# Kernel tuning notes

Hardware: AMD Instinct MI355X
Metric: run time of the kernel (lower is better)

The kernel has to match this reference:

```python
import jax, jax.numpy as jnp
import numpy as np

D_MODEL = 512
D_STATE = 64
LN_EPS = 1e-3  # Keras LayerNormalization default epsilon


def setup_inputs() -> dict:
    key = jax.random.key(0)
    ks = jax.random.split(key, 12)
    B, S, D, N = 8, 4096, D_MODEL, D_STATE

    def glorot(k, shape):
        fan_in, fan_out = shape[0], shape[1]
        lim = np.sqrt(6.0 / (fan_in + fan_out)).astype(np.float32)
        return jax.random.uniform(k, shape, jnp.float32, -lim, lim)

    return {
        "x": jax.random.normal(ks[0], (B, S, D), jnp.float32),
        "ln_gamma": jnp.ones((D,), jnp.float32),
        "ln_beta": jnp.zeros((D,), jnp.float32),
        "W_in": glorot(ks[1], (D, D)),
        "b_in": jnp.zeros((D,), jnp.float32),
        "W_xs": glorot(ks[2], (D, N)),
        "W_B": glorot(ks[3], (D, N)),
        "b_B": jnp.zeros((N,), jnp.float32),
        "W_C": glorot(ks[4], (D, N)),
        "b_C": jnp.zeros((N,), jnp.float32),
        "A_log": jax.random.uniform(ks[5], (N,), jnp.float32, -4.0, -1.0),
        "D_skip": jnp.ones((D,), jnp.float32),
        "W_so": glorot(ks[6], (N, D)),
        "W_out": glorot(ks[7], (D, D)),
        "b_out": jnp.zeros((D,), jnp.float32),
    }


def reference(x, ln_gamma, ln_beta, W_in, b_in, W_xs, W_B, b_B, W_C, b_C,
              A_log, D_skip, W_so, W_out, b_out):
    residual = x
    # LayerNorm over last axis (Keras default eps=1e-3)
    mu = jnp.mean(x, axis=-1, keepdims=True)
    var = jnp.mean(jnp.square(x - mu), axis=-1, keepdims=True)
    xn = (x - mu) * jax.lax.rsqrt(var + LN_EPS) * ln_gamma + ln_beta
    # input projection (this projected x is what feeds the D skip too)
    xp = xn @ W_in + b_in                      # [B, S, D]
    Bmat = xp @ W_B + b_B                      # [B, S, N] selective B(x)
    Cmat = xp @ W_C + b_C                      # [B, S, N] selective C(x)
    xs = xp @ W_xs                             # [B, S, N]
    A_bar = jnp.exp(-jnp.exp(A_log))           # [N], stable decay in (0,1)
    Bx = Bmat * xs                             # per-step drive B_t * x_state_t

    # sequential scan: h_t = A_bar * h_{t-1} + Bx_t
    def step(h, bx):
        h = A_bar * h + bx
        return h, h

    h0 = jnp.zeros((x.shape[0], A_log.shape[0]), x.dtype)
    _, hs = jax.lax.scan(step, h0, jnp.swapaxes(Bx, 0, 1))  # hs: [S, B, N]
    hs = jnp.swapaxes(hs, 0, 1)                             # [B, S, N]

    y = jnp.einsum('bsn,nd->bsd', Cmat * hs, W_so) + D_skip * xp
    y = y @ W_out + b_out
    # dropout is identity at inference (training=None)
    return y + residual
```

## Files before the change

kernel.cpp:

```cpp
#include <hip/hip_runtime.h>
#include <cstdint>
#include <cstddef>


typedef unsigned short bf16_t;
typedef __attribute__((ext_vector_type(8))) short bh8;
typedef __attribute__((ext_vector_type(4))) float f4;

#define M_ROWS 32768
#define SCAN_L 32
#define SCAN_C 128

__device__ __forceinline__ unsigned short f2bf(float f) {
  union { float f; unsigned int u; } c; c.f = f;
  unsigned int u = c.u;
  return (unsigned short)((u + 0x7FFFu + ((u >> 16) & 1u)) >> 16);
}

__device__ __forceinline__ uint2 pack4bf(f4 a) {
  uint2 r;
  r.x = (unsigned)f2bf(a[0]) | ((unsigned)f2bf(a[1]) << 16);
  r.y = (unsigned)f2bf(a[2]) | ((unsigned)f2bf(a[3]) << 16);
  return r;
}

__device__ __forceinline__ void async_cp16(void* lds, const void* g) {
  __builtin_amdgcn_global_load_lds((const __attribute__((address_space(1))) void*)g,
                                   (__attribute__((address_space(3))) void*)lds, 16, 0, 0);
}

__global__ __launch_bounds__(256) void prep_all(
    const float* __restrict__ W_in, const float* __restrict__ W_out,
    const float* __restrict__ W_so, const float* __restrict__ W_xs,
    const float* __restrict__ W_B,  const float* __restrict__ W_C,
    const float* __restrict__ b_in, const float* __restrict__ D_skip,
    const float* __restrict__ A_log,
    bf16_t* __restrict__ Wbig, bf16_t* __restrict__ Wout_t,
    bf16_t* __restrict__ Win_b, bf16_t* __restrict__ Wso_b,
    bf16_t* __restrict__ Wcat_t, bf16_t* __restrict__ Wcat2,
    float* __restrict__ Abar, float* __restrict__ Apow) {
  int i = blockIdx.x * 256 + threadIdx.x;
  if (i < 262144) { int k = i >> 9, n = i & 511;
    Wbig[(size_t)n * 512 + k] = f2bf(W_in[k * 512 + n]); return; }
  i -= 262144;
  if (i < 262144) { int k = i >> 9, n = i & 511;
    Wout_t[(size_t)n * 512 + k] = f2bf(W_out[k * 512 + n]); return; }
  i -= 262144;
  if (i < 262144) { Win_b[i] = f2bf(W_in[i]); return; }
  i -= 262144;
  if (i < 65536) { int r = i >> 9, j = i & 511;
    Win_b[(size_t)(512 + r) * 512 + j] = (r == 0) ? f2bf(b_in[j]) : (bf16_t)0; return; }
  i -= 65536;
  if (i < 65536) { int k = i >> 9, j = i & 511;
    Wso_b[i] = (k < 64) ? f2bf(W_so[k * 512 + j]) : (bf16_t)0; return; }
  i -= 65536;
  if (i < 131072) { int k = i >> 8, n = i & 255;
    float v = 0.f;
    if (n < 64)       v = W_xs[k * 64 + n];
    else if (n < 128) v = W_B[k * 64 + n - 64];
    else if (n < 192) v = W_C[k * 64 + n - 128];
    Wcat_t[(size_t)n * 512 + k] = f2bf(v); return; }
  i -= 131072;
  if (i < 262144) { int k2 = i >> 9, n = i & 511;
    Wcat2[(size_t)n * 576 + 64 + k2] = f2bf(D_skip[k2] * W_out[(size_t)k2 * 512 + n]);
    return; }
  i -= 262144;
  if (i < 32768) { int r = i >> 9, d = i & 511;
    Wbig[(size_t)(704 + r) * 512 + d] = 0; return; }
  i -= 32768;
  if (i < 64) {
    float a = __expf(A_log[i]);
    Abar[i] = __expf(-a);
    Apow[i] = __expf(-a * (float)SCAN_L);
  }
}

__global__ __launch_bounds__(256, 4) void gemm_prep(
    const bf16_t* __restrict__ Win_b, const bf16_t* __restrict__ Wcat_t,
    const bf16_t* __restrict__ Wso_b, const bf16_t* __restrict__ Wout_t,
    const float* __restrict__ b_B, const float* __restrict__ b_C,
    bf16_t* __restrict__ Wbig, bf16_t* __restrict__ Wcat2,
    float* __restrict__ biasp) {
  __shared__ __align__(16) bf16_t As[128 * 64];
  __shared__ __align__(16) bf16_t Bs[128 * 64];
  const int tid = threadIdx.x;
  const int wave = tid >> 6, lane = tid & 63;
  const int quad = lane >> 4, l16 = lane & 15;
  const int wm = (wave >> 1) * 64, wn = (wave & 1) * 64;
  const bool roleW = (blockIdx.x >= 10);
  const int mb = roleW ? 0 : (blockIdx.x >> 1);
  const int nb = roleW ? (blockIdx.x - 10) : (blockIdx.x & 1);
  const bf16_t* Ap = roleW ? Wso_b : Win_b;
  const bf16_t* Bp = roleW ? Wout_t : Wcat_t;

  f4 acc[4][4];
  #pragma unroll
  for (int i = 0; i < 4; ++i)
    #pragma unroll
    for (int j = 0; j < 4; ++j) acc[i][j] = (f4){0.f, 0.f, 0.f, 0.f};

  for (int kt = 0; kt < 8; ++kt) {
    const int k0 = kt << 6;
    __syncthreads();
    #pragma unroll
    for (int i = 0; i < 4; ++i) {
      const int base = (wave * 4 + i) * 64;
      const int cid = base + lane;
      const int row = cid >> 3;
      const int g = (cid & 7) ^ (row & 7);
      async_cp16((char*)As + base * 16,
                 Ap + (size_t)(mb * 128 + row) * 512 + k0 + g * 8);
    }
    #pragma unroll
    for (int i = 0; i < 4; ++i) {
      const int base = (wave * 4 + i) * 64;
      const int cid = base + lane;
      const int row = cid >> 3;
      const int g = (cid & 7) ^ (row & 7);
      async_cp16((char*)Bs + base * 16,
                 Bp + (size_t)(nb * 128 + row) * 512 + k0 + g * 8);
    }
    __syncthreads();
    #pragma unroll
    for (int ks = 0; ks < 2; ++ks) {
      const int gb = ks * 4 + quad;
      bh8 af[4], bfv[4];
      #pragma unroll
      for (int im = 0; im < 4; ++im) {
        const int row = wm + im * 16 + l16;
        af[im] = *(const bh8*)((const char*)As + row * 128 + ((gb ^ (row & 7)) * 16));
      }
      #pragma unroll
      for (int in_ = 0; in_ < 4; ++in_) {
        const int row = wn + in_ * 16 + l16;
        bfv[in_] = *(const bh8*)((const char*)Bs + row * 128 + ((gb ^ (row & 7)) * 16));
      }
      #pragma unroll
      for (int im = 0; im < 4; ++im)
        #pragma unroll
        for (int in_ = 0; in_ < 4; ++in_)
          acc[im][in_] = __builtin_amdgcn_mfma_f32_16x16x32_bf16(af[im], bfv[in_],
                                                                 acc[im][in_], 0, 0, 0);
    }
  }

  #pragma unroll
  for (int im = 0; im < 4; ++im) {
    #pragma unroll
    for (int in_ = 0; in_ < 4; ++in_) {
      const int row0 = mb * 128 + wm + im * 16 + quad * 4;
      const int col = nb * 128 + wn + in_ * 16 + l16;
      if (roleW) {
        if (row0 < 64)
          *(uint2*)(Wcat2 + (size_t)col * 576 + row0) = pack4bf(acc[im][in_]);
      } else if (col < 192) {
        if (row0 < 512) {
          *(uint2*)(Wbig + (size_t)(512 + col) * 512 + row0) = pack4bf(acc[im][in_]);
        } else if (row0 == 512) {
          float v = acc[im][in_][0];
          if (col >= 128)     v += b_C[col - 128];
          else if (col >= 64) v += b_B[col - 64];
          biasp[col] = v;
        }
      }
    }
  }
}

__global__ __launch_bounds__(256) void ln_kernel(
    const float* __restrict__ x, const float* __restrict__ gamma,
    const float* __restrict__ beta, bf16_t* __restrict__ xn) {
  const int row = blockIdx.x * 4 + (threadIdx.x >> 6);
  const int lane = threadIdx.x & 63;
  const float* xr = x + (size_t)row * 512 + lane * 8;
  float4 v0 = *(const float4*)xr;
  float4 v1 = *(const float4*)(xr + 4);
  float s  = v0.x + v0.y + v0.z + v0.w + v1.x + v1.y + v1.z + v1.w;
  float sq = v0.x*v0.x + v0.y*v0.y + v0.z*v0.z + v0.w*v0.w
           + v1.x*v1.x + v1.y*v1.y + v1.z*v1.z + v1.w*v1.w;
  #pragma unroll
  for (int off = 32; off > 0; off >>= 1) {
    s  += __shfl_xor(s, off, 64);
    sq += __shfl_xor(sq, off, 64);
  }
  const float mu  = s * (1.0f / 512.0f);
  const float var = sq * (1.0f / 512.0f) - mu * mu;
  const float rs  = rsqrtf(var + 1e-3f);
  float4 g0 = *(const float4*)(gamma + lane * 8);
  float4 g1 = *(const float4*)(gamma + lane * 8 + 4);
  float4 b0 = *(const float4*)(beta + lane * 8);
  float4 b1 = *(const float4*)(beta + lane * 8 + 4);
  bh8 ov;
  ov[0] = (short)f2bf((v0.x - mu) * rs * g0.x + b0.x);
  ov[1] = (short)f2bf((v0.y - mu) * rs * g0.y + b0.y);
  ov[2] = (short)f2bf((v0.z - mu) * rs * g0.z + b0.z);
  ov[3] = (short)f2bf((v0.w - mu) * rs * g0.w + b0.w);
  ov[4] = (short)f2bf((v1.x - mu) * rs * g1.x + b1.x);
  ov[5] = (short)f2bf((v1.y - mu) * rs * g1.y + b1.y);
  ov[6] = (short)f2bf((v1.z - mu) * rs * g1.z + b1.z);
  ov[7] = (short)f2bf((v1.w - mu) * rs * g1.w + b1.w);
  *(bh8*)(xn + (size_t)row * 512 + lane * 8) = ov;
}

template <int MODE>
__global__ __launch_bounds__(256, 4) void gemm_mfma(
    const bf16_t* __restrict__ A0, const bf16_t* __restrict__ A1,
    const bf16_t* __restrict__ Wt, int K,
    bf16_t* __restrict__ outbf, float* __restrict__ outf,
    const float* __restrict__ bias0, const float* __restrict__ bias1,
    const float* __restrict__ resid) {
  __shared__ __align__(16) bf16_t As[128 * 64];
  __shared__ __align__(16) bf16_t Bs[128 * 64];
  const int tid = threadIdx.x;
  const int wave = tid >> 6, lane = tid & 63;
  const int quad = lane >> 4, l16 = lane & 15;
  const int wm = (wave >> 1) * 64, wn = (wave & 1) * 64;
  const int mb = blockIdx.x, nb = blockIdx.y;

  f4 acc[4][4];
  #pragma unroll
  for (int i = 0; i < 4; ++i)
    #pragma unroll
    for (int j = 0; j < 4; ++j) acc[i][j] = (f4){0.f, 0.f, 0.f, 0.f};

  const int nkt = K >> 6;
  for (int kt = 0; kt < nkt; ++kt) {
    const int k0 = kt << 6;
    const bf16_t* Ap; int lda, kk;
    if (MODE == 3) {
      if (kt == 0) { Ap = A0; lda = 64;  kk = 0; }
      else         { Ap = A1; lda = 512; kk = k0 - 64; }
    } else { Ap = A0; lda = K; kk = k0; }

    __syncthreads();
    #pragma unroll
    for (int i = 0; i < 4; ++i) {
      const int base = (wave * 4 + i) * 64;
      const int cid = base + lane;
      const int row = cid >> 3;
      const int g = (cid & 7) ^ (row & 7);
      async_cp16((char*)As + base * 16,
                 Ap + (size_t)(mb * 128 + row) * lda + kk + g * 8);
    }
    #pragma unroll
    for (int i = 0; i < 4; ++i) {
      const int base = (wave * 4 + i) * 64;
      const int cid = base + lane;
      const int row = cid >> 3;
      const int g = (cid & 7) ^ (row & 7);
      async_cp16((char*)Bs + base * 16,
                 Wt + (size_t)(nb * 128 + row) * K + k0 + g * 8);
    }
    __syncthreads();

    #pragma unroll
    for (int ks = 0; ks < 2; ++ks) {
      const int gb = ks * 4 + quad;
      bh8 af[4], bfv[4];
      #pragma unroll
      for (int im = 0; im < 4; ++im) {
        const int row = wm + im * 16 + l16;
        af[im] = *(const bh8*)((const char*)As + row * 128 + ((gb ^ (row & 7)) * 16));
      }
      #pragma unroll
      for (int in_ = 0; in_ < 4; ++in_) {
        const int row = wn + in_ * 16 + l16;
        bfv[in_] = *(const bh8*)((const char*)Bs + row * 128 + ((gb ^ (row & 7)) * 16));
      }
      #pragma unroll
      for (int im = 0; im < 4; ++im)
        #pragma unroll
        for (int in_ = 0; in_ < 4; ++in_)
          acc[im][in_] = __builtin_amdgcn_mfma_f32_16x16x32_bf16(af[im], bfv[in_],
                                                                 acc[im][in_], 0, 0, 0);
    }
  }

  #pragma unroll
  for (int im = 0; im < 4; ++im) {
    #pragma unroll
    for (int in_ = 0; in_ < 4; ++in_) {
      #pragma unroll
      for (int r = 0; r < 4; ++r) {
        const int row = mb * 128 + wm + im * 16 + quad * 4 + r;
        const int col = nb * 128 + wn + in_ * 16 + l16;
        float v = acc[im][in_][r];
        if (MODE == 2) {
          if (col < 512) {
            outbf[(size_t)row * 512 + col] = f2bf(v + bias0[col]);
          } else if (col < 704) {
            const int cc = col - 512;
            outf[((size_t)(cc >> 6) * M_ROWS + row) * 64 + (cc & 63)] = v + bias1[cc];
          }
        } else {
          outf[(size_t)row * 512 + col] = v + bias0[col] + resid[(size_t)row * 512 + col];
        }
      }
    }
  }
}

__global__ __launch_bounds__(64) void scan_chunk(
    const float* __restrict__ projP, const float* __restrict__ Abar,
    float* __restrict__ carry) {
  const int b = blockIdx.x >> 7, c = blockIdx.x & (SCAN_C - 1), n = threadIdx.x;
  const float A = Abar[n];
  const size_t row0 = (size_t)b * 4096 + c * SCAN_L;
  const float* pxs = projP + row0 * 64;
  const float* pB  = projP + ((size_t)M_ROWS + row0) * 64;
  float h = 0.f;
  for (int i = 0; i < SCAN_L; ++i)
    h = fmaf(A, h, pxs[i * 64 + n] * pB[i * 64 + n]);
  carry[(b * SCAN_C + c) * 64 + n] = h;
}

__global__ __launch_bounds__(512) void scan_carry(
    const float* __restrict__ carry, const float* __restrict__ Apow,
    float* __restrict__ cin) {
  const int b = threadIdx.x >> 6, n = threadIdx.x & 63;
  const float Ap = Apow[n];
  float h = 0.f;
  for (int c = 0; c < SCAN_C; ++c) {
    cin[(b * SCAN_C + c) * 64 + n] = h;
    h = fmaf(Ap, h, carry[(b * SCAN_C + c) * 64 + n]);
  }
}

__global__ __launch_bounds__(64) void scan_apply(
    const float* __restrict__ projP, const float* __restrict__ Abar,
    const float* __restrict__ cin, bf16_t* __restrict__ CH) {
  const int b = blockIdx.x >> 7, c = blockIdx.x & (SCAN_C - 1), n = threadIdx.x;
  const float A = Abar[n];
  const size_t row0 = (size_t)b * 4096 + c * SCAN_L;
  const float* pxs = projP + row0 * 64;
  const float* pB  = projP + ((size_t)M_ROWS + row0) * 64;
  const float* pC  = projP + ((size_t)2 * M_ROWS + row0) * 64;
  bf16_t* o = CH + row0 * 64;
  float h = cin[(b * SCAN_C + c) * 64 + n];
  for (int i = 0; i < SCAN_L; ++i) {
    h = fmaf(A, h, pxs[i * 64 + n] * pB[i * 64 + n]);
    o[i * 64 + n] = f2bf(pC[i * 64 + n] * h);
  }
}

extern "C" void kernel_launch(void* const* d_in, const int* in_sizes, int n_in,
                              void* d_out, int out_size, void* d_ws, size_t ws_size,
                              hipStream_t stream) {
  const float* x      = (const float*)d_in[0];
  const float* ln_g   = (const float*)d_in[1];
  const float* ln_b   = (const float*)d_in[2];
  const float* W_in   = (const float*)d_in[3];
  const float* b_in   = (const float*)d_in[4];
  const float* W_xs   = (const float*)d_in[5];
  const float* W_B    = (const float*)d_in[6];
  const float* b_B    = (const float*)d_in[7];
  const float* W_C    = (const float*)d_in[8];
  const float* b_C    = (const float*)d_in[9];
  const float* A_log  = (const float*)d_in[10];
  const float* D_skip = (const float*)d_in[11];
  const float* W_so   = (const float*)d_in[12];
  const float* W_out  = (const float*)d_in[13];
  const float* b_out  = (const float*)d_in[14];
  float* out = (float*)d_out;

  char* w = (char*)d_ws;
  auto carve = [&](size_t bytes) {
    char* p = w; w += (bytes + 255) & ~(size_t)255; return p;
  };
  bf16_t* xn     = (bf16_t*)carve((size_t)M_ROWS * 512 * 2);
  bf16_t* xp     = (bf16_t*)carve((size_t)M_ROWS * 512 * 2);
  float*  projP  = (float*)carve((size_t)3 * M_ROWS * 64 * 4);
  bf16_t* CH     = (bf16_t*)carve((size_t)M_ROWS * 64 * 2);
  float*  carry  = (float*)carve((size_t)8 * SCAN_C * 64 * 4);
  float*  cin    = (float*)carve((size_t)8 * SCAN_C * 64 * 4);
  bf16_t* Wbig   = (bf16_t*)carve((size_t)768 * 512 * 2);
  bf16_t* Wcat2  = (bf16_t*)carve((size_t)512 * 576 * 2);
  bf16_t* Win_b  = (bf16_t*)carve((size_t)640 * 512 * 2);
  bf16_t* Wso_b  = (bf16_t*)carve((size_t)128 * 512 * 2);
  bf16_t* Wout_t = (bf16_t*)carve((size_t)512 * 512 * 2);
  bf16_t* Wcat_t = (bf16_t*)carve((size_t)256 * 512 * 2);
  float*  biasp  = (float*)carve(192 * 4);
  float*  Abar   = (float*)carve(256);
  float*  Apow   = (float*)carve(256);

  prep_all<<<5249, 256, 0, stream>>>(W_in, W_out, W_so, W_xs, W_B, W_C, b_in,
                                     D_skip, A_log, Wbig, Wout_t, Win_b, Wso_b,
                                     Wcat_t, Wcat2, Abar, Apow);
  gemm_prep<<<14, 256, 0, stream>>>(Win_b, Wcat_t, Wso_b, Wout_t, b_B, b_C,
                                    Wbig, Wcat2, biasp);
  ln_kernel<<<8192, 256, 0, stream>>>(x, ln_g, ln_b, xn);
  gemm_mfma<2><<<dim3(256, 6), 256, 0, stream>>>(xn, nullptr, Wbig, 512,
                                                 xp, projP, b_in, biasp, nullptr);
  scan_chunk<<<8 * SCAN_C, 64, 0, stream>>>(projP, Abar, carry);
  scan_carry<<<1, 512, 0, stream>>>(carry, Apow, cin);
  scan_apply<<<8 * SCAN_C, 64, 0, stream>>>(projP, Abar, cin, CH);
  gemm_mfma<3><<<dim3(256, 4), 256, 0, stream>>>(CH, xp, Wcat2, 576,
                                                 nullptr, out, b_out, nullptr, x);
}
```

Before: 267.7 us.

## Fold W_in into D-skip output weights and merge scan carry into apply

Precomposes W_in with D_skip*W_out so the final GEMM reads the normalized input xn directly instead of a materialized xp. The first GEMM then only produces the 192 projection columns, which removes the 512-column bf16 xp write and its later re-read. The separate single-block scan_carry kernel is dropped. Each scan_apply block now recomputes its chunk's carry-in with a serial loop over a transposed carry array, which adds up to 128 dependent FMAs per thread. Composing W_in with the skip weights in bf16 changes rounding slightly.

Result: faster. 238.5 us (-10.9%).

```diff
diff --git a/kernel.cpp b/kernel.cpp
--- a/kernel.cpp
+++ b/kernel.cpp
@@ -35,16 +35,16 @@
     const float* __restrict__ W_B,  const float* __restrict__ W_C,
     const float* __restrict__ b_in, const float* __restrict__ D_skip,
     const float* __restrict__ A_log,
-    bf16_t* __restrict__ Wbig, bf16_t* __restrict__ Wout_t,
+    bf16_t* __restrict__ Wout_t, bf16_t* __restrict__ Wdout_t,
     bf16_t* __restrict__ Win_b, bf16_t* __restrict__ Wso_b,
-    bf16_t* __restrict__ Wcat_t, bf16_t* __restrict__ Wcat2,
+    bf16_t* __restrict__ Wcat_t, bf16_t* __restrict__ Wproj,
     float* __restrict__ Abar, float* __restrict__ Apow) {
   int i = blockIdx.x * 256 + threadIdx.x;
   if (i < 262144) { int k = i >> 9, n = i & 511;
-    Wbig[(size_t)n * 512 + k] = f2bf(W_in[k * 512 + n]); return; }
+    Wout_t[(size_t)n * 512 + k] = f2bf(W_out[k * 512 + n]); return; }
   i -= 262144;
   if (i < 262144) { int k = i >> 9, n = i & 511;
-    Wout_t[(size_t)n * 512 + k] = f2bf(W_out[k * 512 + n]); return; }
+    Wdout_t[(size_t)n * 512 + k] = f2bf(D_skip[k] * W_out[k * 512 + n]); return; }
   i -= 262144;
   if (i < 262144) { Win_b[i] = f2bf(W_in[i]); return; }
   i -= 262144;
@@ -61,12 +61,8 @@
     else if (n < 192) v = W_C[k * 64 + n - 128];
     Wcat_t[(size_t)n * 512 + k] = f2bf(v); return; }
   i -= 131072;
-  if (i < 262144) { int k2 = i >> 9, n = i & 511;
-    Wcat2[(size_t)n * 576 + 64 + k2] = f2bf(D_skip[k2] * W_out[(size_t)k2 * 512 + n]);
-    return; }
-  i -= 262144;
   if (i < 32768) { int r = i >> 9, d = i & 511;
-    Wbig[(size_t)(704 + r) * 512 + d] = 0; return; }
+    Wproj[(size_t)(192 + r) * 512 + d] = 0; return; }
   i -= 32768;
   if (i < 64) {
     float a = __expf(A_log[i]);
@@ -78,20 +74,22 @@
 __global__ __launch_bounds__(256, 4) void gemm_prep(
     const bf16_t* __restrict__ Win_b, const bf16_t* __restrict__ Wcat_t,
     const bf16_t* __restrict__ Wso_b, const bf16_t* __restrict__ Wout_t,
+    const bf16_t* __restrict__ Wdout_t,
     const float* __restrict__ b_B, const float* __restrict__ b_C,
-    bf16_t* __restrict__ Wbig, bf16_t* __restrict__ Wcat2,
-    float* __restrict__ biasp) {
+    bf16_t* __restrict__ Wproj, bf16_t* __restrict__ Wcat2,
+    float* __restrict__ biasp, float* __restrict__ biasW2) {
   __shared__ __align__(16) bf16_t As[128 * 64];
   __shared__ __align__(16) bf16_t Bs[128 * 64];
   const int tid = threadIdx.x;
   const int wave = tid >> 6, lane = tid & 63;
   const int quad = lane >> 4, l16 = lane & 15;
   const int wm = (wave >> 1) * 64, wn = (wave & 1) * 64;
-  const bool roleW = (blockIdx.x >= 10);
-  const int mb = roleW ? 0 : (blockIdx.x >> 1);
-  const int nb = roleW ? (blockIdx.x - 10) : (blockIdx.x & 1);
-  const bf16_t* Ap = roleW ? Wso_b : Win_b;
-  const bf16_t* Bp = roleW ? Wout_t : Wcat_t;
+  int role, mb, nb;
+  if (blockIdx.x < 10)      { role = 0; mb = blockIdx.x >> 1; nb = blockIdx.x & 1; }
+  else if (blockIdx.x < 14) { role = 1; mb = 0; nb = blockIdx.x - 10; }
+  else { role = 2; int t = blockIdx.x - 14; mb = t >> 2; nb = t & 3; }
+  const bf16_t* Ap = (role == 1) ? Wso_b : Win_b;
+  const bf16_t* Bp = (role == 0) ? Wcat_t : (role == 1) ? Wout_t : Wdout_t;
 
   f4 acc[4][4];
   #pragma unroll
@@ -150,17 +148,25 @@
     for (int in_ = 0; in_ < 4; ++in_) {
       const int row0 = mb * 128 + wm + im * 16 + quad * 4;
       const int col = nb * 128 + wn + in_ * 16 + l16;
-      if (roleW) {
+      if (role == 0) {
+        if (col < 192) {
+          if (row0 < 512) {
+            *(uint2*)(Wproj + (size_t)col * 512 + row0) = pack4bf(acc[im][in_]);
+          } else if (row0 == 512) {
+            float v = acc[im][in_][0];
+            if (col >= 128)     v += b_C[col - 128];
+            else if (col >= 64) v += b_B[col - 64];
+            biasp[col] = v;
+          }
+        }
+      } else if (role == 1) {
         if (row0 < 64)
           *(uint2*)(Wcat2 + (size_t)col * 576 + row0) = pack4bf(acc[im][in_]);
-      } else if (col < 192) {
+      } else {
         if (row0 < 512) {
-          *(uint2*)(Wbig + (size_t)(512 + col) * 512 + row0) = pack4bf(acc[im][in_]);
+          *(uint2*)(Wcat2 + (size_t)col * 576 + 64 + row0) = pack4bf(acc[im][in_]);
         } else if (row0 == 512) {
-          float v = acc[im][in_][0];
-          if (col >= 128)     v += b_C[col - 128];
-          else if (col >= 64) v += b_B[col - 64];
-          biasp[col] = v;
+          biasW2[col] = acc[im][in_][0];
         }
       }
     }
@@ -206,7 +212,7 @@
 __global__ __launch_bounds__(256, 4) void gemm_mfma(
     const bf16_t* __restrict__ A0, const bf16_t* __restrict__ A1,
     const bf16_t* __restrict__ Wt, int K,
-    bf16_t* __restrict__ outbf, float* __restrict__ outf,
+    float* __restrict__ outf,
     const float* __restrict__ bias0, const float* __restrict__ bias1,
     const float* __restrict__ resid) {
   __shared__ __align__(16) bf16_t As[128 * 64];
@@ -286,14 +292,11 @@
         const int col = nb * 128 + wn + in_ * 16 + l16;
         float v = acc[im][in_][r];
         if (MODE == 2) {
-          if (col < 512) {
-            outbf[(size_t)row * 512 + col] = f2bf(v + bias0[col]);
-          } else if (col < 704) {
-            const int cc = col - 512;
-            outf[((size_t)(cc >> 6) * M_ROWS + row) * 64 + (cc & 63)] = v + bias1[cc];
-          }
+          if (col < 192)
+            outf[((size_t)(col >> 6) * M_ROWS + row) * 64 + (col & 63)] = v + bias1[col];
         } else {
-          outf[(size_t)row * 512 + col] = v + bias0[col] + resid[(size_t)row * 512 + col];
+          outf[(size_t)row * 512 + col] =
+              v + bias0[col] + bias1[col] + resid[(size_t)row * 512 + col];
         }
       }
     }
@@ -302,7 +305,7 @@
 
 __global__ __launch_bounds__(64) void scan_chunk(
     const float* __restrict__ projP, const float* __restrict__ Abar,
-    float* __restrict__ carry) {
+    float* __restrict__ carryT) {
   const int b = blockIdx.x >> 7, c = blockIdx.x & (SCAN_C - 1), n = threadIdx.x;
   const float A = Abar[n];
   const size_t row0 = (size_t)b * 4096 + c * SCAN_L;
@@ -311,32 +314,24 @@
   float h = 0.f;
   for (int i = 0; i < SCAN_L; ++i)
     h = fmaf(A, h, pxs[i * 64 + n] * pB[i * 64 + n]);
-  carry[(b * SCAN_C + c) * 64 + n] = h;
-}
-
-__global__ __launch_bounds__(512) void scan_carry(
-    const float* __restrict__ carry, const float* __restrict__ Apow,
-    float* __restrict__ cin) {
-  const int b = threadIdx.x >> 6, n = threadIdx.x & 63;
-  const float Ap = Apow[n];
-  float h = 0.f;
-  for (int c = 0; c < SCAN_C; ++c) {
-    cin[(b * SCAN_C + c) * 64 + n] = h;
-    h = fmaf(Ap, h, carry[(b * SCAN_C + c) * 64 + n]);
-  }
+  carryT[((size_t)(b * 64 + n)) * SCAN_C + c] = h;
 }
 
 __global__ __launch_bounds__(64) void scan_apply(
     const float* __restrict__ projP, const float* __restrict__ Abar,
-    const float* __restrict__ cin, bf16_t* __restrict__ CH) {
+    const float* __restrict__ Apow, const float* __restrict__ carryT,
+    bf16_t* __restrict__ CH) {
   const int b = blockIdx.x >> 7, c = blockIdx.x & (SCAN_C - 1), n = threadIdx.x;
   const float A = Abar[n];
+  const float Ap = Apow[n];
+  const float* cr = carryT + ((size_t)(b * 64 + n)) * SCAN_C;
+  float h = 0.f;
+  for (int j = 0; j < c; ++j) h = fmaf(Ap, h, cr[j]);
   const size_t row0 = (size_t)b * 4096 + c * SCAN_L;
   const float* pxs = projP + row0 * 64;
   const float* pB  = projP + ((size_t)M_ROWS + row0) * 64;
   const float* pC  = projP + ((size_t)2 * M_ROWS + row0) * 64;
   bf16_t* o = CH + row0 * 64;
-  float h = cin[(b * SCAN_C + c) * 64 + n];
   for (int i = 0; i < SCAN_L; ++i) {
     h = fmaf(A, h, pxs[i * 64 + n] * pB[i * 64 + n]);
     o[i * 64 + n] = f2bf(pC[i * 64 + n] * h);
@@ -368,32 +363,31 @@
     char* p = w; w += (bytes + 255) & ~(size_t)255; return p;
   };
   bf16_t* xn     = (bf16_t*)carve((size_t)M_ROWS * 512 * 2);
-  bf16_t* xp     = (bf16_t*)carve((size_t)M_ROWS * 512 * 2);
   float*  projP  = (float*)carve((size_t)3 * M_ROWS * 64 * 4);
   bf16_t* CH     = (bf16_t*)carve((size_t)M_ROWS * 64 * 2);
-  float*  carry  = (float*)carve((size_t)8 * SCAN_C * 64 * 4);
-  float*  cin    = (float*)carve((size_t)8 * SCAN_C * 64 * 4);
-  bf16_t* Wbig   = (bf16_t*)carve((size_t)768 * 512 * 2);
+  float*  carryT = (float*)carve((size_t)8 * 64 * SCAN_C * 4);
+  bf16_t* Wproj  = (bf16_t*)carve((size_t)256 * 512 * 2);
   bf16_t* Wcat2  = (bf16_t*)carve((size_t)512 * 576 * 2);
   bf16_t* Win_b  = (bf16_t*)carve((size_t)640 * 512 * 2);
   bf16_t* Wso_b  = (bf16_t*)carve((size_t)128 * 512 * 2);
   bf16_t* Wout_t = (bf16_t*)carve((size_t)512 * 512 * 2);
+  bf16_t* Wdout_t= (bf16_t*)carve((size_t)512 * 512 * 2);
   bf16_t* Wcat_t = (bf16_t*)carve((size_t)256 * 512 * 2);
   float*  biasp  = (float*)carve(192 * 4);
+  float*  biasW2 = (float*)carve(512 * 4);
   float*  Abar   = (float*)carve(256);
   float*  Apow   = (float*)carve(256);
 
-  prep_all<<<5249, 256, 0, stream>>>(W_in, W_out, W_so, W_xs, W_B, W_C, b_in,
-                                     D_skip, A_log, Wbig, Wout_t, Win_b, Wso_b,
-                                     Wcat_t, Wcat2, Abar, Apow);
-  gemm_prep<<<14, 256, 0, stream>>>(Win_b, Wcat_t, Wso_b, Wout_t, b_B, b_C,
-                                    Wbig, Wcat2, biasp);
+  prep_all<<<4227, 256, 0, stream>>>(W_in, W_out, W_so, W_xs, W_B, W_C, b_in,
+                                     D_skip, A_log, Wout_t, Wdout_t, Win_b,
+                                     Wso_b, Wcat_t, Wproj, Abar, Apow);
+  gemm_prep<<<34, 256, 0, stream>>>(Win_b, Wcat_t, Wso_b, Wout_t, Wdout_t,
+                                    b_B, b_C, Wproj, Wcat2, biasp, biasW2);
   ln_kernel<<<8192, 256, 0, stream>>>(x, ln_g, ln_b, xn);
-  gemm_mfma<2><<<dim3(256, 6), 256, 0, stream>>>(xn, nullptr, Wbig, 512,
-                                                 xp, projP, b_in, biasp, nullptr);
-  scan_chunk<<<8 * SCAN_C, 64, 0, stream>>>(projP, Abar, carry);
-  scan_carry<<<1, 512, 0, stream>>>(carry, Apow, cin);
-  scan_apply<<<8 * SCAN_C, 64, 0, stream>>>(projP, Abar, cin, CH);
-  gemm_mfma<3><<<dim3(256, 4), 256, 0, stream>>>(CH, xp, Wcat2, 576,
-                                                 nullptr, out, b_out, nullptr, x);
-}
+  gemm_mfma<2><<<dim3(256, 2), 256, 0, stream>>>(xn, nullptr, Wproj, 512,
+                                                 projP, nullptr, biasp, nullptr);
+  scan_chunk<<<8 * SCAN_C, 64, 0, stream>>>(projP, Abar, carryT);
+  scan_apply<<<8 * SCAN_C, 64, 0, stream>>>(projP, Abar, Apow, carryT, CH);
+  gemm_mfma<3><<<dim3(256, 4), 256, 0, stream>>>(CH, xn, Wcat2, 576,
+                                                 out, b_out, biasW2, x);
+}
```
